# Kernel tuning notes

Hardware: AMD Instinct MI355X
Metric: run time of the kernel (lower is better)

The kernel has to match this reference:

```python
import jax, jax.numpy as jnp
import numpy as np

B, N, D, K = 32, 4096, 256, 16
EPS = 1e-12  # F.normalize default eps


def setup_inputs() -> dict:
    key = jax.random.key(0)
    k1, k2, k3, k4, k5 = jax.random.split(key, 5)
    x = jax.random.normal(k1, (B, N, D), dtype=jnp.float32)
    mask = jax.random.randint(k2, (B, N), 0, 2).astype(bool)
    W = jax.random.normal(k3, (K, D), dtype=jnp.float32) * 0.02
    b = jax.random.normal(k4, (K,), dtype=jnp.float32) * 0.02
    centroids = jax.random.normal(k5, (K, D), dtype=jnp.float32) * 0.02
    return {"x": x, "mask": mask, "W": W, "b": b, "centroids": centroids}


def reference(x, mask, W, b, centroids):
    # logits: (B, N, K); masked tokens get -1e9 on every cluster
    logits = jnp.einsum('bnd,kd->bnk', x, W) + b
    logits = jnp.where(mask[..., None], logits, jnp.float32(-1e9))
    assign = jax.nn.softmax(logits, axis=-1) * mask[..., None].astype(x.dtype)
    # vlad[b,k,:] = sum_n assign[b,n,k] * (x[b,n,:] - c[k,:])
    #            = (assign^T @ x) - (sum_n assign) * c   (avoids (B,N,K,D) tensor)
    vlad = jnp.einsum('bnk,bnd->bkd', assign, x) \
           - jnp.sum(assign, axis=1)[..., None] * centroids[None]
    # intra-cluster L2 normalize (dim=2)
    vlad = vlad / jnp.maximum(jnp.linalg.norm(vlad, axis=2, keepdims=True), EPS)
    vlad = vlad.reshape(x.shape[0], K * D)
    # global L2 normalize (dim=1)
    return vlad / jnp.maximum(jnp.linalg.norm(vlad, axis=1, keepdims=True), EPS)
```

## Files before the change

### kernel.cpp

```cpp
#include <hip/hip_runtime.h>
#include <cstdint>
#include <cstddef>

#define BB 32
#define NN 4096
#define DD 256
#define KK 16

constexpr float FEPS = 1e-12f;

__device__ __forceinline__ float dot4(float4 a, float4 b) {
  return a.x*b.x + a.y*b.y + a.z*b.z + a.w*b.w;
}
__device__ __forceinline__ float4 f4add(float4 a, float4 b) {
  return make_float4(a.x+b.x, a.y+b.y, a.z+b.z, a.w+b.w);
}
__device__ __forceinline__ float4 f4fma(float s, float4 x, float4 a) {
  a.x += s*x.x; a.y += s*x.y; a.z += s*x.z; a.w += s*x.w; return a;
}

template <int TILE>
__global__ __launch_bounds__(256, (TILE == 64 ? 8 : 4)) void fused_kernel(
    const float* __restrict__ x, const int* __restrict__ mask,
    const float* __restrict__ W, const float* __restrict__ bias,
    float* __restrict__ outv, float* __restrict__ outs, int partial_mode)
{
  constexpr int NG    = 256 / TILE;
  constexpr int KPT   = KK / NG;
  constexpr int SW4   = TILE / 64;
  constexpr int WPG   = 4 / NG;
  constexpr int TPBAT = NN / TILE;

  __shared__ float4 xs4[2][TILE * 5];
  __shared__ float  al[TILE * KK];
  __shared__ float  psum[TILE][NG];
  __shared__ float  asacc[WPG][KK];

  const int tid  = threadIdx.x;
  const int lane = tid & 63;
  const int wave = tid >> 6;
  const int tok  = tid & (TILE - 1);
  const int kg   = __builtin_amdgcn_readfirstlane(tid / TILE);
  const int slot = __builtin_amdgcn_readfirstlane(wave & (WPG - 1));

  const int tile = blockIdx.x;
  const int b    = tile / TPBAT;
  const int n0   = (tile % TPBAT) * TILE;

  const float4* xb4 = reinterpret_cast<const float4*>(x + ((size_t)b*NN + n0)*DD);
  const int*    mb  = mask + (size_t)b*NN + n0;

  float part[KPT];
#pragma unroll
  for (int q = 0; q < KPT; ++q) part[q] = bias[kg * KPT + q];

  const int st = tid >> 2;
  const int sj = tid & 3;

  {
    float4 pre[SW4];
#pragma unroll
    for (int l = 0; l < SW4; ++l)
      pre[l] = xb4[(size_t)(st + l * 64) * 64 + sj];
#pragma unroll
    for (int l = 0; l < SW4; ++l)
      xs4[0][(st + l * 64) * 5 + sj] = pre[l];
  }

#pragma unroll 1
  for (int c = 0; c < 16; ++c) {
    __syncthreads();
    const int cur = c & 1;

    float4 nxt[SW4];
    if (c < 15) {
#pragma unroll
      for (int l = 0; l < SW4; ++l)
        nxt[l] = xb4[(size_t)(st + l * 64) * 64 + (c + 1) * 4 + sj];
    }

#pragma unroll
    for (int j = 0; j < 4; ++j) {
      const float4 xv = xs4[cur][tok * 5 + j];
      const float* Wc = W + c * 16 + j * 4;
#pragma unroll
      for (int q = 0; q < KPT; ++q) {
        const float4 wv = *reinterpret_cast<const float4*>(Wc + (kg * KPT + q) * DD);
        part[q] += dot4(xv, wv);
      }
    }

    if (c < 15) {
#pragma unroll
      for (int l = 0; l < SW4; ++l)
        xs4[cur ^ 1][(st + l * 64) * 5 + sj] = nxt[l];
    }
  }

  float e[KPT], pexp = 0.f;
#pragma unroll
  for (int q = 0; q < KPT; ++q) { e[q] = __expf(part[q]); pexp += e[q]; }
  psum[tok][kg] = pexp;
  __syncthreads();
  float a[KPT];
  {
    float denom = 0.f;
#pragma unroll
    for (int g = 0; g < NG; ++g) denom += psum[tok][g];
    const float r = mb[tok] ? (1.0f / denom) : 0.0f;
#pragma unroll
    for (int q = 0; q < KPT; ++q) a[q] = e[q] * r;
#pragma unroll
    for (int q4 = 0; q4 < KPT; q4 += 4)
      *reinterpret_cast<float4*>(&al[tok * KK + kg * KPT + q4]) =
          make_float4(a[q4], a[q4+1], a[q4+2], a[q4+3]);
  }

  {
    float red[KPT];
#pragma unroll
    for (int q = 0; q < KPT; ++q) red[q] = a[q];
#pragma unroll
    for (int off = 32; off >= 1; off >>= 1)
#pragma unroll
      for (int q = 0; q < KPT; ++q) red[q] += __shfl_xor(red[q], off);
    if (lane == 0)
#pragma unroll
      for (int q = 0; q < KPT; ++q) asacc[slot][kg * KPT + q] = red[q];
  }
  __syncthreads();

  float4 acc0 = make_float4(0.f,0.f,0.f,0.f);
  float4 acc1 = make_float4(0.f,0.f,0.f,0.f);
  float4 acc2 = make_float4(0.f,0.f,0.f,0.f);
  float4 acc3 = make_float4(0.f,0.f,0.f,0.f);

  const float4* xw = xb4 + lane;
  const int kq4 = 4 * wave;

  float4 w0 = xw[0], w1 = xw[64], w2 = xw[128], w3 = xw[192];

#pragma unroll 4
  for (int t = 0; t < TILE - 4; ++t) {
    const float4 nx = xw[(size_t)(t + 4) * 64];
    const float4 av = *reinterpret_cast<const float4*>(&al[t * KK + kq4]);
    acc0 = f4fma(av.x, w0, acc0);
    acc1 = f4fma(av.y, w0, acc1);
    acc2 = f4fma(av.z, w0, acc2);
    acc3 = f4fma(av.w, w0, acc3);
    w0 = w1; w1 = w2; w2 = w3; w3 = nx;
  }
#pragma unroll
  for (int t = TILE - 4; t < TILE; ++t) {
    const float4 av = *reinterpret_cast<const float4*>(&al[t * KK + kq4]);
    acc0 = f4fma(av.x, w0, acc0);
    acc1 = f4fma(av.y, w0, acc1);
    acc2 = f4fma(av.z, w0, acc2);
    acc3 = f4fma(av.w, w0, acc3);
    w0 = w1; w1 = w2; w2 = w3;
  }

  const int kq = wave * 4;
  if (partial_mode) {
    float4* dst = reinterpret_cast<float4*>(outv + (size_t)tile * KK * DD);
    dst[(kq + 0) * 64 + lane] = acc0;
    dst[(kq + 1) * 64 + lane] = acc1;
    dst[(kq + 2) * 64 + lane] = acc2;
    dst[(kq + 3) * 64 + lane] = acc3;
    if (tid < KK) {
      float s = 0.f;
#pragma unroll
      for (int sl = 0; sl < WPG; ++sl) s += asacc[sl][tid];
      outs[tile * KK + tid] = s;
    }
  } else {
    float* vb = outv + (size_t)b * KK * DD;
    const float4 aa4[4] = {acc0, acc1, acc2, acc3};
#pragma unroll
    for (int i = 0; i < 4; ++i) {
      float* p = vb + (kq + i) * DD + 4 * lane;
      atomicAdd(p + 0, aa4[i].x);
      atomicAdd(p + 1, aa4[i].y);
      atomicAdd(p + 2, aa4[i].z);
      atomicAdd(p + 3, aa4[i].w);
    }
    if (tid < KK) {
      float s = 0.f;
#pragma unroll
      for (int sl = 0; sl < WPG; ++sl) s += asacc[sl][tid];
      atomicAdd(&outs[b * KK + tid], s);
    }
  }
}

__global__ __launch_bounds__(256) void finalizeA_kernel(
    const float* __restrict__ pv, const float* __restrict__ ps,
    const float* __restrict__ cent, float* __restrict__ vtmp,
    float* __restrict__ ssbuf, int nslice)
{
  const int blk = blockIdx.x;
  const int b   = blk >> 4;
  const int k   = blk & 15;
  const int tid = threadIdx.x;
  const int sg  = tid >> 6;
  const int ld  = tid & 63;

  __shared__ float4 cmbA[3][64];

  float pval = 0.f;
  for (int s = ld; s < nslice; s += 64)
    pval += ps[(size_t)(b * nslice + s) * KK + k];
#pragma unroll
  for (int off = 32; off >= 1; off >>= 1) pval += __shfl_xor(pval, off);
  const float ssum = pval;

  const float4* pv4 = reinterpret_cast<const float4*>(pv);
  const size_t base = ((size_t)b * nslice * KK + k) * 64 + ld;
  float4 a0 = make_float4(0.f,0.f,0.f,0.f), a1 = a0, a2 = a0, a3 = a0;
  int s = sg;
  for (; s + 12 < nslice; s += 16) {
    a0 = f4add(a0, pv4[base + (size_t)(s     ) * (KK * 64)]);
    a1 = f4add(a1, pv4[base + (size_t)(s +  4) * (KK * 64)]);
    a2 = f4add(a2, pv4[base + (size_t)(s +  8) * (KK * 64)]);
    a3 = f4add(a3, pv4[base + (size_t)(s + 12) * (KK * 64)]);
  }
  for (; s < nslice; s += 4)
    a0 = f4add(a0, pv4[base + (size_t)s * (KK * 64)]);
  float4 tot = f4add(f4add(a0, a1), f4add(a2, a3));

  if (sg > 0) cmbA[sg - 1][ld] = tot;
  __syncthreads();

  if (sg == 0) {
    tot = f4add(tot, f4add(cmbA[0][ld], f4add(cmbA[1][ld], cmbA[2][ld])));
    const float4 cv = reinterpret_cast<const float4*>(cent)[k * 64 + ld];
    float4 v;
    v.x = tot.x - ssum * cv.x;
    v.y = tot.y - ssum * cv.y;
    v.z = tot.z - ssum * cv.z;
    v.w = tot.w - ssum * cv.w;
    reinterpret_cast<float4*>(vtmp)[((size_t)b * KK + k) * 64 + ld] = v;
    float p = dot4(v, v);
#pragma unroll
    for (int off = 32; off >= 1; off >>= 1) p += __shfl_xor(p, off);
    if (ld == 0) ssbuf[blk] = p;
  }
}

__global__ __launch_bounds__(1024) void finalizeB_kernel(
    const float* __restrict__ vtmp, const float* __restrict__ ssbuf,
    float* __restrict__ out)
{
  const int b    = blockIdx.x;
  const int tid  = threadIdx.x;
  const int d    = tid & 255;
  const int kq   = tid >> 8;
  const int lane = tid & 63;
  const int w    = tid >> 6;

  __shared__ float redB[16];
  __shared__ float gsh;

  float u[4];
  float p2 = 0.f;
#pragma unroll
  for (int kk = 0; kk < 4; ++kk) {
    const int k = kq * 4 + kk;
    const float rk = 1.0f / fmaxf(sqrtf(ssbuf[b * KK + k]), FEPS);
    u[kk] = vtmp[((size_t)b * KK + k) * DD + d] * rk;
    p2 += u[kk] * u[kk];
  }
#pragma unroll
  for (int off = 32; off >= 1; off >>= 1) p2 += __shfl_xor(p2, off);
  if (lane == 0) redB[w] = p2;
  __syncthreads();

  if (tid == 0) {
    float g = 0.f;
#pragma unroll
    for (int i = 0; i < 16; ++i) g += redB[i];
    gsh = 1.0f / fmaxf(sqrtf(g), FEPS);
  }
  __syncthreads();

  const float g = gsh;
#pragma unroll
  for (int kk = 0; kk < 4; ++kk) {
    const int k = kq * 4 + kk;
    out[(size_t)b * KK * DD + k * DD + d] = u[kk] * g;
  }
}

extern "C" void kernel_launch(void* const* d_in, const int* in_sizes, int n_in,
                              void* d_out, int out_size, void* d_ws, size_t ws_size,
                              hipStream_t stream) {
  const float* x    = (const float*)d_in[0];
  const int*   mask = (const int*)d_in[1];
  const float* W    = (const float*)d_in[2];
  const float* bias = (const float*)d_in[3];
  const float* cent = (const float*)d_in[4];
  float* out = (float*)d_out;

  const size_t vtmpN = (size_t)BB * KK * DD;
  const size_t ssN   = (size_t)BB * KK;

  const size_t t64   = (size_t)BB * (NN / 64);
  const size_t t128  = (size_t)BB * (NN / 128);
  const size_t need64  = (t64  * KK * DD + t64  * KK + vtmpN + ssN) * sizeof(float);
  const size_t need128 = (t128 * KK * DD + t128 * KK + vtmpN + ssN) * sizeof(float);

  if (ws_size >= need64) {
    float* pv    = (float*)d_ws;
    float* ps    = pv + t64 * KK * DD;
    float* vtmp  = ps + t64 * KK;
    float* ssbuf = vtmp + vtmpN;
    fused_kernel<64><<<(int)t64, 256, 0, stream>>>(x, mask, W, bias, pv, ps, 1);
    finalizeA_kernel<<<BB * KK, 256, 0, stream>>>(pv, ps, cent, vtmp, ssbuf, NN / 64);
    finalizeB_kernel<<<BB, 1024, 0, stream>>>(vtmp, ssbuf, out);
  } else if (ws_size >= need128) {
    float* pv    = (float*)d_ws;
    float* ps    = pv + t128 * KK * DD;
    float* vtmp  = ps + t128 * KK;
    float* ssbuf = vtmp + vtmpN;
    fused_kernel<128><<<(int)t128, 256, 0, stream>>>(x, mask, W, bias, pv, ps, 1);
    finalizeA_kernel<<<BB * KK, 256, 0, stream>>>(pv, ps, cent, vtmp, ssbuf, NN / 128);
    finalizeB_kernel<<<BB, 1024, 0, stream>>>(vtmp, ssbuf, out);
  } else {
    float* vacc  = (float*)d_ws;
    float* sacc  = vacc + vtmpN;
    float* vtmp  = sacc + ssN;
    float* ssbuf = vtmp + vtmpN;
    hipMemsetAsync(d_ws, 0, (vtmpN + ssN) * sizeof(float), stream);
    fused_kernel<64><<<(int)t64, 256, 0, stream>>>(x, mask, W, bias, vacc, sacc, 0);
    finalizeA_kernel<<<BB * KK, 256, 0, stream>>>(vacc, sacc, cent, vtmp, ssbuf, 1);
    finalizeB_kernel<<<BB, 1024, 0, stream>>>(vtmp, ssbuf, out);
  }
}
```

Baseline: 63.05 us.

## Compact unmasked tokens per tile and skip loads and math for masked ones

Builds a per-tile compaction map of unmasked tokens with a wave ballot and popcount, then loads and processes only those rows in both the logits GEMV and the assign^T·x accumulation. Masked tokens contribute exactly zero, so skipping them removes roughly half of the global x traffic and FMA work for random masks. In exchange it adds an extra barrier and an indirect gather through shared memory. It also drops the explicit 4-deep register prefetch in the accumulation loop in favour of a variable-trip loop.

```diff
diff --git a/kernel.cpp b/kernel.cpp
--- a/kernel.cpp
+++ b/kernel.cpp
@@ -35,6 +35,7 @@
   __shared__ float  al[TILE * KK];
   __shared__ float  psum[TILE][NG];
   __shared__ float  asacc[WPG][KK];
+  __shared__ int    cmap[TILE];
 
   const int tid  = threadIdx.x;
   const int lane = tid & 63;
@@ -50,6 +51,21 @@
   const float4* xb4 = reinterpret_cast<const float4*>(x + ((size_t)b*NN + n0)*DD);
   const int*    mb  = mask + (size_t)b*NN + n0;
 
+  int cnt;
+  if constexpr (TILE == 64) {
+    const int m = mb[lane];
+    const unsigned long long bits = __ballot(m != 0);
+    cnt = __builtin_amdgcn_readfirstlane((int)__popcll(bits));
+    if (wave == 0 && m) {
+      const unsigned long long below = bits & ((1ull << lane) - 1ull);
+      cmap[(int)__popcll(below)] = lane;
+    }
+  } else {
+    cnt = TILE;
+    if (tid < TILE) cmap[tid] = tid;
+  }
+  __syncthreads();
+
   float part[KPT];
 #pragma unroll
   for (int q = 0; q < KPT; ++q) part[q] = bias[kg * KPT + q];
@@ -57,14 +73,20 @@
   const int st = tid >> 2;
   const int sj = tid & 3;
 
-  {
-    float4 pre[SW4];
-#pragma unroll
-    for (int l = 0; l < SW4; ++l)
-      pre[l] = xb4[(size_t)(st + l * 64) * 64 + sj];
-#pragma unroll
-    for (int l = 0; l < SW4; ++l)
-      xs4[0][(st + l * 64) * 5 + sj] = pre[l];
+  int srow[SW4], sact[SW4];
+#pragma unroll
+  for (int l = 0; l < SW4; ++l) {
+    const int sl = st + l * 64;
+    sact[l] = sl < cnt;
+    srow[l] = sact[l] ? cmap[sl] : 0;
+  }
+
+#pragma unroll
+  for (int l = 0; l < SW4; ++l) {
+    if (sact[l]) {
+      const float4 p0 = xb4[(size_t)srow[l] * 64 + sj];
+      xs4[0][(st + l * 64) * 5 + sj] = p0;
+    }
   }
 
 #pragma unroll 1
@@ -76,7 +98,8 @@
     if (c < 15) {
 #pragma unroll
       for (int l = 0; l < SW4; ++l)
-        nxt[l] = xb4[(size_t)(st + l * 64) * 64 + (c + 1) * 4 + sj];
+        if (sact[l])
+          nxt[l] = xb4[(size_t)srow[l] * 64 + (c + 1) * 4 + sj];
     }
 
 #pragma unroll
@@ -93,13 +116,22 @@
     if (c < 15) {
 #pragma unroll
       for (int l = 0; l < SW4; ++l)
-        xs4[cur ^ 1][(st + l * 64) * 5 + sj] = nxt[l];
-    }
-  }
+        if (sact[l])
+          xs4[cur ^ 1][(st + l * 64) * 5 + sj] = nxt[l];
+    }
+  }
+
+  int act;
+  if constexpr (TILE == 64) act = (tok < cnt);
+  else                      act = mb[tok];
 
   float e[KPT], pexp = 0.f;
 #pragma unroll
-  for (int q = 0; q < KPT; ++q) { e[q] = __expf(part[q]); pexp += e[q]; }
+  for (int q = 0; q < KPT; ++q) {
+    const float ev = __expf(part[q]);
+    e[q] = act ? ev : 0.0f;
+    pexp += e[q];
+  }
   psum[tok][kg] = pexp;
   __syncthreads();
   float a[KPT];
@@ -107,7 +139,7 @@
     float denom = 0.f;
 #pragma unroll
     for (int g = 0; g < NG; ++g) denom += psum[tok][g];
-    const float r = mb[tok] ? (1.0f / denom) : 0.0f;
+    const float r = act ? (1.0f / denom) : 0.0f;
 #pragma unroll
     for (int q = 0; q < KPT; ++q) a[q] = e[q] * r;
 #pragma unroll
@@ -138,26 +170,15 @@
   const float4* xw = xb4 + lane;
   const int kq4 = 4 * wave;
 
-  float4 w0 = xw[0], w1 = xw[64], w2 = xw[128], w3 = xw[192];
-
 #pragma unroll 4
-  for (int t = 0; t < TILE - 4; ++t) {
-    const float4 nx = xw[(size_t)(t + 4) * 64];
-    const float4 av = *reinterpret_cast<const float4*>(&al[t * KK + kq4]);
-    acc0 = f4fma(av.x, w0, acc0);
-    acc1 = f4fma(av.y, w0, acc1);
-    acc2 = f4fma(av.z, w0, acc2);
-    acc3 = f4fma(av.w, w0, acc3);
-    w0 = w1; w1 = w2; w2 = w3; w3 = nx;
-  }
-#pragma unroll
-  for (int t = TILE - 4; t < TILE; ++t) {
-    const float4 av = *reinterpret_cast<const float4*>(&al[t * KK + kq4]);
-    acc0 = f4fma(av.x, w0, acc0);
-    acc1 = f4fma(av.y, w0, acc1);
-    acc2 = f4fma(av.z, w0, acc2);
-    acc3 = f4fma(av.w, w0, acc3);
-    w0 = w1; w1 = w2; w2 = w3;
+  for (int tt = 0; tt < cnt; ++tt) {
+    const int tr = cmap[tt];
+    const float4 xv = xw[(size_t)tr * 64];
+    const float4 av = *reinterpret_cast<const float4*>(&al[tt * KK + kq4]);
+    acc0 = f4fma(av.x, xv, acc0);
+    acc1 = f4fma(av.y, xv, acc1);
+    acc2 = f4fma(av.z, xv, acc2);
+    acc3 = f4fma(av.w, xv, acc3);
   }
 
   const int kq = wave * 4;
```

New measurement: 58.58 us, median of 3. 1.08x faster.
